# Kernel tuning notes

Hardware: AMD Instinct MI355X
Metric: run time of the kernel (lower is better)

Reference implementation:

```python
import jax, jax.numpy as jnp
import numpy as np

TEMPERATURE = 0.07
EPS = 1e-20

def setup_inputs() -> dict:
    key = jax.random.key(0)
    k1, k2 = jax.random.split(key)
    B, D, L = 4096, 256, 20
    features = jax.random.normal(k1, (B, D), dtype=jnp.float32)
    labels = jax.random.randint(k2, (B, L), 0, 5)
    return {"features": features, "labels": labels}

def reference(features, labels):
    B = features.shape[0]
    dt = features.dtype
    # [B, B] similarity logits, numerically stabilized (max is detached in torch)
    logits = (features @ features.T) / TEMPERATURE
    logits = logits - jax.lax.stop_gradient(jnp.max(logits, axis=1, keepdims=True))
    logits_mask = 1.0 - jnp.eye(B, dtype=dt)  # exclude self-contrast
    # shared across all label columns (the torch loop recomputes this each iter)
    exp_sum = jnp.sum(jnp.exp(logits) * logits_mask, axis=1, keepdims=True)
    log_prob = logits - jnp.log(exp_sum + EPS)

    def per_label(carry, lab):  # lab: [B] labels for one time-step
        mask = (lab[:, None] == lab[None, :]).astype(dt) * logits_mask  # [B, B]
        pos = mask.sum(1)                                   # positives per anchor
        single = (pos == 0).astype(dt)                      # anchors with no positives
        mean_lp = (mask * log_prob).sum(1) / (pos + single)
        loss_vec = -mean_lp * (1.0 - single)
        loss_i = loss_vec.sum() / (jnp.asarray(B, dt) - single.sum())
        return carry, loss_i

    _, losses = jax.lax.scan(per_label, jnp.float32(0.0), labels.T)  # [L]
    # torch fills minute_loss[:, i] with the scalar loss_i, then takes mean -> mean over i
    return jnp.mean(losses)
```

## Files before the change

### kernel.cpp

```cpp
#include <hip/hip_runtime.h>


#define B_N 4096
#define D_K 256
#define L_N 20
#define INVT 14.285714285714286f

#define FB_OFF   0x000000u
#define C_OFF    0x200000u
#define CNT_OFF  0x204000u
#define WT_OFF   0x210000u
#define MP_OFF   0x230000u
#define EP_OFF   0x330000u
#define NN_OFF   0x430000u
#define LP_OFF   0x630000u
#define SP_OFF   0x630500u

typedef __bf16 bf16x8 __attribute__((ext_vector_type(8)));
typedef float f32x4 __attribute__((ext_vector_type(4)));

struct __align__(16) U4 { unsigned int x, y, z, w; };

__device__ __forceinline__ unsigned int f2bf(float x) {
  unsigned int u = __float_as_uint(x);
  return (u + 0x7FFFu + ((u >> 16) & 1u)) >> 16;
}

__global__ __launch_bounds__(256) void k_prep(const float* __restrict__ F,
                                              const int* __restrict__ lab,
                                              unsigned char* __restrict__ ws) {
  __shared__ int sc[4][5];
  const int bid = blockIdx.x, t = threadIdx.x;
  if (bid < 1024) {
    const int w = t >> 6, l = t & 63;
    const int row = bid * 4 + w;
    float4 v = *(const float4*)(F + row * 256 + l * 4);
    float ss = v.x * v.x + v.y * v.y + v.z * v.z + v.w * v.w;
    #pragma unroll
    for (int off = 1; off < 64; off <<= 1) ss += __shfl_xor(ss, off, 64);
    ushort4 pk;
    pk.x = (unsigned short)f2bf(v.x);
    pk.y = (unsigned short)f2bf(v.y);
    pk.z = (unsigned short)f2bf(v.z);
    pk.w = (unsigned short)f2bf(v.w);
    *(ushort4*)(ws + FB_OFF + (row * 256 + l * 4) * 2) = pk;
    if (l == 0) ((float*)(ws + C_OFF))[row] = ss * INVT;
  } else if (bid < 1044) {
    const int l = bid - 1024;
    int c0 = 0, c1 = 0, c2 = 0, c3 = 0, c4 = 0;
    for (int j = t; j < B_N; j += 256) {
      int v = lab[j * L_N + l];
      c0 += (v == 0); c1 += (v == 1); c2 += (v == 2); c3 += (v == 3); c4 += (v == 4);
    }
    #pragma unroll
    for (int off = 1; off < 64; off <<= 1) {
      c0 += __shfl_xor(c0, off, 64); c1 += __shfl_xor(c1, off, 64);
      c2 += __shfl_xor(c2, off, 64); c3 += __shfl_xor(c3, off, 64);
      c4 += __shfl_xor(c4, off, 64);
    }
    const int w = t >> 6;
    if ((t & 63) == 0) { sc[w][0] = c0; sc[w][1] = c1; sc[w][2] = c2; sc[w][3] = c3; sc[w][4] = c4; }
    __syncthreads();
    if (t < 5) ((int*)(ws + CNT_OFF))[l * 5 + t] = sc[0][t] + sc[1][t] + sc[2][t] + sc[3][t];
  } else {
    const int idx = bid - 1044;
    const int l = idx >> 4, chunk = idx & 15;
    const int d = t;
    float a0 = 0, a1 = 0, a2 = 0, a3 = 0, a4 = 0;
    const int j0 = chunk * 256;
    for (int j = j0; j < j0 + 256; ++j) {
      int v = lab[j * L_N + l];
      float x = F[j * 256 + d];
      a0 += (v == 0) ? x : 0.f;
      a1 += (v == 1) ? x : 0.f;
      a2 += (v == 2) ? x : 0.f;
      a3 += (v == 3) ? x : 0.f;
      a4 += (v == 4) ? x : 0.f;
    }
    float* Wt = (float*)(ws + WT_OFF);
    atomicAdd(Wt + (l * 5 + 0) * 256 + d, a0);
    atomicAdd(Wt + (l * 5 + 1) * 256 + d, a1);
    atomicAdd(Wt + (l * 5 + 2) * 256 + d, a2);
    atomicAdd(Wt + (l * 5 + 3) * 256 + d, a3);
    atomicAdd(Wt + (l * 5 + 4) * 256 + d, a4);
  }
}

__global__ __launch_bounds__(512, 2) void k_main(unsigned char* __restrict__ ws) {
  __shared__ unsigned char smem[65536];
  const int bid = blockIdx.x, t = threadIdx.x;
  const int w = t >> 6, l = t & 63;
  const int lr = l & 15, lg = l >> 4;
  const unsigned char* fbB = ws + FB_OFF;
  const bool isN = (bid >= 256);
  int rowbase, colb;
  if (!isN) {
    const int bm = bid & 7, bn = bid >> 3;
    rowbase = bm * 512 + w * 64;
    colb = bn * 128;
    const int srow = t >> 2, q = t & 3;
    const unsigned char* src = fbB + (colb + srow) * 512 + q * 128;
    #pragma unroll
    for (int i = 0; i < 8; ++i) {
      U4 v = *(const U4*)(src + i * 16);
      const int kb = q * 128 + i * 16;
      *(U4*)(smem + srow * 512 + (kb ^ ((srow & 7) << 4))) = v;
    }
  } else {
    rowbase = (bid - 256) * 512 + w * 64;
    colb = -(1 << 20);
    const float* Wt = (const float*)(ws + WT_OFF);
    for (int s = 0; s < 8; ++s) {
      const int rid = t + s * 512;
      const int srow = rid >> 5, k0 = (rid & 31) * 8;
      float4 f0 = *(const float4*)(Wt + srow * 256 + k0);
      float4 f1 = *(const float4*)(Wt + srow * 256 + k0 + 4);
      U4 pk;
      pk.x = f2bf(f0.x) | (f2bf(f0.y) << 16);
      pk.y = f2bf(f0.z) | (f2bf(f0.w) << 16);
      pk.z = f2bf(f1.x) | (f2bf(f1.y) << 16);
      pk.w = f2bf(f1.z) | (f2bf(f1.w) << 16);
      *(U4*)(smem + srow * 512 + ((k0 * 2) ^ ((srow & 7) << 4))) = pk;
    }
  }
  bf16x8 afr[4][8];
  #pragma unroll
  for (int mi = 0; mi < 4; ++mi)
    #pragma unroll
    for (int kk = 0; kk < 8; ++kk) {
      U4 va = *(const U4*)(fbB + (rowbase + mi * 16 + lr) * 512 + kk * 64 + lg * 16);
      afr[mi][kk] = __builtin_bit_cast(bf16x8, va);
    }
  __syncthreads();
  const float* cvec = (const float*)(ws + C_OFF);
  float* MP = (float*)(ws + MP_OFF);
  float* EP = (float*)(ws + EP_OFF);
  float* NN = (float*)(ws + NN_OFF);
  #pragma unroll 1
  for (int tile = 0; tile < 2; ++tile) {
    f32x4 acc[4][4] = {};
    #pragma unroll
    for (int kk = 0; kk < 8; ++kk) {
      bf16x8 bfr[4];
      #pragma unroll
      for (int n = 0; n < 4; ++n) {
        const int brow = tile * 64 + n * 16 + lr;
        const int kb = kk * 64 + lg * 16;
        bfr[n] = __builtin_bit_cast(bf16x8,
            *(const U4*)(smem + brow * 512 + (kb ^ ((brow & 7) << 4))));
      }
      #pragma unroll
      for (int mi = 0; mi < 4; ++mi)
        #pragma unroll
        for (int n = 0; n < 4; ++n)
          acc[mi][n] = __builtin_amdgcn_mfma_f32_16x16x32_bf16(afr[mi][kk], bfr[n], acc[mi][n], 0, 0, 0);
    }
    if (!isN) {
      #pragma unroll
      for (int mi = 0; mi < 4; ++mi) {
        #pragma unroll
        for (int r = 0; r < 4; ++r) {
          const int row = rowbase + mi * 16 + lg * 4 + r;
          const float crow = cvec[row];
          float vm = -3.4e38f, es = 0.f;
          #pragma unroll
          for (int n = 0; n < 4; ++n) {
            const int col = colb + tile * 64 + n * 16 + lr;
            const float v = acc[mi][n][r] * INVT;
            vm = fmaxf(vm, v);
            const float e = __expf(v - crow);
            es += (col == row) ? 0.f : e;
          }
          #pragma unroll
          for (int off = 1; off < 16; off <<= 1) {
            vm = fmaxf(vm, __shfl_xor(vm, off, 16));
            es += __shfl_xor(es, off, 16);
          }
          if (lr == 0) {
            const int c2 = (colb >> 6) + tile;
            MP[row * 64 + c2] = vm;
            EP[row * 64 + c2] = es;
          }
        }
      }
    } else {
      #pragma unroll
      for (int mi = 0; mi < 4; ++mi)
        #pragma unroll
        for (int n = 0; n < 4; ++n) {
          const int col = tile * 64 + n * 16 + lr;
          #pragma unroll
          for (int r = 0; r < 4; ++r) {
            const int row = rowbase + mi * 16 + lg * 4 + r;
            NN[row * 128 + col] = acc[mi][n][r];
          }
        }
    }
  }
}

__global__ __launch_bounds__(256) void k_final(const int* __restrict__ lab,
                                               unsigned char* __restrict__ ws) {
  __shared__ float sL[4][20], sS[4][20];
  const int t = threadIdx.x;
  const int i = blockIdx.x * 256 + t;
  const float* MP = (const float*)(ws + MP_OFF);
  const float* EP = (const float*)(ws + EP_OFF);
  const float* NNv = (const float*)(ws + NN_OFF);
  const float* cvec = (const float*)(ws + C_OFF);
  const int* cnts = (const int*)(ws + CNT_OFF);
  float m = -3.4e38f, e = 0.f;
  #pragma unroll
  for (int k = 0; k < 16; ++k) {
    float4 mv = *(const float4*)(MP + i * 64 + k * 4);
    float4 ev = *(const float4*)(EP + i * 64 + k * 4);
    m = fmaxf(m, fmaxf(fmaxf(mv.x, mv.y), fmaxf(mv.z, mv.w)));
    e += ev.x + ev.y + ev.z + ev.w;
  }
  const float ci = cvec[i];
  const float lp = logf(e * __expf(ci - m) + 1e-20f);
  const int w = t >> 6, lane = t & 63;
  for (int ll = 0; ll < 20; ++ll) {
    const int v = lab[i * 20 + ll];
    const int cnt = cnts[ll * 5 + v] - 1;
    float lv = 0.f, sg = 0.f;
    if (cnt > 0) {
      const float me = NNv[i * 128 + ll * 5 + v] * INVT - ci;
      const float ss = me - (float)cnt * m;
      lv = lp - ss / (float)cnt;
    } else {
      sg = 1.f;
    }
    #pragma unroll
    for (int off = 1; off < 64; off <<= 1) {
      lv += __shfl_xor(lv, off, 64);
      sg += __shfl_xor(sg, off, 64);
    }
    if (lane == 0) { sL[w][ll] = lv; sS[w][ll] = sg; }
  }
  __syncthreads();
  if (t < 20) {
    ((float*)(ws + LP_OFF))[blockIdx.x * 20 + t] = sL[0][t] + sL[1][t] + sL[2][t] + sL[3][t];
    ((float*)(ws + SP_OFF))[blockIdx.x * 20 + t] = sS[0][t] + sS[1][t] + sS[2][t] + sS[3][t];
  }
}

__global__ void k_out(unsigned char* __restrict__ ws, float* __restrict__ out) {
  const int t = threadIdx.x;
  float v = 0.f;
  if (t < 20) {
    const float* LPp = (const float*)(ws + LP_OFF);
    const float* SPp = (const float*)(ws + SP_OFF);
    float Ls = 0.f, Ss = 0.f;
    for (int b = 0; b < 16; ++b) { Ls += LPp[b * 20 + t]; Ss += SPp[b * 20 + t]; }
    v = Ls / (4096.f - Ss);
  }
  #pragma unroll
  for (int off = 1; off < 64; off <<= 1) v += __shfl_xor(v, off, 64);
  if (t == 0) out[0] = v * 0.05f;
}

extern "C" void kernel_launch(void* const* d_in, const int* in_sizes, int n_in,
                              void* d_out, int out_size, void* d_ws, size_t ws_size,
                              hipStream_t stream) {
  const float* F = (const float*)d_in[0];
  const int* lab = (const int*)d_in[1];
  unsigned char* ws = (unsigned char*)d_ws;
  float* out = (float*)d_out;
  hipMemsetAsync(ws + WT_OFF, 0, 128 * 256 * 4, stream);
  k_prep<<<1364, 256, 0, stream>>>(F, lab, ws);
  k_main<<<264, 512, 0, stream>>>(ws);
  k_final<<<16, 256, 0, stream>>>(lab, ws);
  k_out<<<1, 64, 0, stream>>>(ws, out);
}
```

Before: 160.2 us.

## Replace atomic class-sum accumulation with partial buffers and transpose row-stat partials

The per-label class feature sums now go to four per-chunk partial buffers with plain stores, which the N-blocks of k_main add together. This removes the memset launch and the float atomics. Each block now loops over 1024 rows instead of 256, so fewer blocks run in that phase. The per-tile row max and exp-sum partials are staged in shared memory and written column-major, so stores from k_main and loads in k_final become coalesced, at the cost of extra LDS space per block.

```diff
diff --git a/kernel.cpp b/kernel.cpp
--- a/kernel.cpp
+++ b/kernel.cpp
@@ -9,12 +9,12 @@
 #define FB_OFF   0x000000u
 #define C_OFF    0x200000u
 #define CNT_OFF  0x204000u
-#define WT_OFF   0x210000u
-#define MP_OFF   0x230000u
-#define EP_OFF   0x330000u
-#define NN_OFF   0x430000u
-#define LP_OFF   0x630000u
-#define SP_OFF   0x630500u
+#define WP_OFF   0x210000u
+#define MPT_OFF  0x290000u
+#define EPT_OFF  0x390000u
+#define NN_OFF   0x490000u
+#define LP_OFF   0x690000u
+#define SP_OFF   0x690500u
 
 typedef __bf16 bf16x8 __attribute__((ext_vector_type(8)));
 typedef float f32x4 __attribute__((ext_vector_type(4)));
@@ -64,11 +64,11 @@
     if (t < 5) ((int*)(ws + CNT_OFF))[l * 5 + t] = sc[0][t] + sc[1][t] + sc[2][t] + sc[3][t];
   } else {
     const int idx = bid - 1044;
-    const int l = idx >> 4, chunk = idx & 15;
+    const int l = idx >> 2, chunk = idx & 3;
     const int d = t;
     float a0 = 0, a1 = 0, a2 = 0, a3 = 0, a4 = 0;
-    const int j0 = chunk * 256;
-    for (int j = j0; j < j0 + 256; ++j) {
+    const int j0 = chunk * 1024;
+    for (int j = j0; j < j0 + 1024; ++j) {
       int v = lab[j * L_N + l];
       float x = F[j * 256 + d];
       a0 += (v == 0) ? x : 0.f;
@@ -77,17 +77,17 @@
       a3 += (v == 3) ? x : 0.f;
       a4 += (v == 4) ? x : 0.f;
     }
-    float* Wt = (float*)(ws + WT_OFF);
-    atomicAdd(Wt + (l * 5 + 0) * 256 + d, a0);
-    atomicAdd(Wt + (l * 5 + 1) * 256 + d, a1);
-    atomicAdd(Wt + (l * 5 + 2) * 256 + d, a2);
-    atomicAdd(Wt + (l * 5 + 3) * 256 + d, a3);
-    atomicAdd(Wt + (l * 5 + 4) * 256 + d, a4);
+    float* WPc = (float*)(ws + WP_OFF) + chunk * (128 * 256);
+    WPc[(l * 5 + 0) * 256 + d] = a0;
+    WPc[(l * 5 + 1) * 256 + d] = a1;
+    WPc[(l * 5 + 2) * 256 + d] = a2;
+    WPc[(l * 5 + 3) * 256 + d] = a3;
+    WPc[(l * 5 + 4) * 256 + d] = a4;
   }
 }
 
 __global__ __launch_bounds__(512, 2) void k_main(unsigned char* __restrict__ ws) {
-  __shared__ unsigned char smem[65536];
+  __shared__ unsigned char smem[65536 + 8192];
   const int bid = blockIdx.x, t = threadIdx.x;
   const int w = t >> 6, l = t & 63;
   const int lr = l & 15, lg = l >> 4;
@@ -109,12 +109,22 @@
   } else {
     rowbase = (bid - 256) * 512 + w * 64;
     colb = -(1 << 20);
-    const float* Wt = (const float*)(ws + WT_OFF);
+    const float* WP = (const float*)(ws + WP_OFF);
     for (int s = 0; s < 8; ++s) {
       const int rid = t + s * 512;
       const int srow = rid >> 5, k0 = (rid & 31) * 8;
-      float4 f0 = *(const float4*)(Wt + srow * 256 + k0);
-      float4 f1 = *(const float4*)(Wt + srow * 256 + k0 + 4);
+      float4 f0 = make_float4(0.f, 0.f, 0.f, 0.f);
+      float4 f1 = make_float4(0.f, 0.f, 0.f, 0.f);
+      if (srow < 100) {
+        #pragma unroll
+        for (int c = 0; c < 4; ++c) {
+          const float* p = WP + c * 32768 + srow * 256 + k0;
+          float4 g0 = *(const float4*)p;
+          float4 g1 = *(const float4*)(p + 4);
+          f0.x += g0.x; f0.y += g0.y; f0.z += g0.z; f0.w += g0.w;
+          f1.x += g1.x; f1.y += g1.y; f1.z += g1.z; f1.w += g1.w;
+        }
+      }
       U4 pk;
       pk.x = f2bf(f0.x) | (f2bf(f0.y) << 16);
       pk.y = f2bf(f0.z) | (f2bf(f0.w) << 16);
@@ -133,8 +143,8 @@
     }
   __syncthreads();
   const float* cvec = (const float*)(ws + C_OFF);
-  float* MP = (float*)(ws + MP_OFF);
-  float* EP = (float*)(ws + EP_OFF);
+  float* MPT = (float*)(ws + MPT_OFF);
+  float* EPT = (float*)(ws + EPT_OFF);
   float* NN = (float*)(ws + NN_OFF);
   #pragma unroll 1
   for (int tile = 0; tile < 2; ++tile) {
@@ -156,6 +166,7 @@
           acc[mi][n] = __builtin_amdgcn_mfma_f32_16x16x32_bf16(afr[mi][kk], bfr[n], acc[mi][n], 0, 0, 0);
     }
     if (!isN) {
+      float2* scr = (float2*)(smem + 65536 + (w * 2 + tile) * 512);
       #pragma unroll
       for (int mi = 0; mi < 4; ++mi) {
         #pragma unroll
@@ -176,13 +187,13 @@
             vm = fmaxf(vm, __shfl_xor(vm, off, 16));
             es += __shfl_xor(es, off, 16);
           }
-          if (lr == 0) {
-            const int c2 = (colb >> 6) + tile;
-            MP[row * 64 + c2] = vm;
-            EP[row * 64 + c2] = es;
-          }
+          if (lr == 0) scr[mi * 16 + lg * 4 + r] = make_float2(vm, es);
         }
       }
+      const float2 v2 = scr[l];
+      const int c2 = (colb >> 6) + tile;
+      MPT[c2 * 4096 + rowbase + l] = v2.x;
+      EPT[c2 * 4096 + rowbase + l] = v2.y;
     } else {
       #pragma unroll
       for (int mi = 0; mi < 4; ++mi)
@@ -204,18 +215,16 @@
   __shared__ float sL[4][20], sS[4][20];
   const int t = threadIdx.x;
   const int i = blockIdx.x * 256 + t;
-  const float* MP = (const float*)(ws + MP_OFF);
-  const float* EP = (const float*)(ws + EP_OFF);
+  const float* MPT = (const float*)(ws + MPT_OFF);
+  const float* EPT = (const float*)(ws + EPT_OFF);
   const float* NNv = (const float*)(ws + NN_OFF);
   const float* cvec = (const float*)(ws + C_OFF);
   const int* cnts = (const int*)(ws + CNT_OFF);
   float m = -3.4e38f, e = 0.f;
   #pragma unroll
-  for (int k = 0; k < 16; ++k) {
-    float4 mv = *(const float4*)(MP + i * 64 + k * 4);
-    float4 ev = *(const float4*)(EP + i * 64 + k * 4);
-    m = fmaxf(m, fmaxf(fmaxf(mv.x, mv.y), fmaxf(mv.z, mv.w)));
-    e += ev.x + ev.y + ev.z + ev.w;
+  for (int c2 = 0; c2 < 64; ++c2) {
+    m = fmaxf(m, MPT[c2 * 4096 + i]);
+    e += EPT[c2 * 4096 + i];
   }
   const float ci = cvec[i];
   const float lp = logf(e * __expf(ci - m) + 1e-20f);
@@ -267,8 +276,7 @@
   const int* lab = (const int*)d_in[1];
   unsigned char* ws = (unsigned char*)d_ws;
   float* out = (float*)d_out;
-  hipMemsetAsync(ws + WT_OFF, 0, 128 * 256 * 4, stream);
-  k_prep<<<1364, 256, 0, stream>>>(F, lab, ws);
+  k_prep<<<1124, 256, 0, stream>>>(F, lab, ws);
   k_main<<<264, 512, 0, stream>>>(ws);
   k_final<<<16, 256, 0, stream>>>(lab, ws);
   k_out<<<1, 64, 0, stream>>>(ws, out);
```

Result: slower. 241.6 us (+50.8%).
